# Optimization experiments

Measured on AMD Instinct MI355X. Metric: run time of the kernel, lower is better.

The kernel has to match this reference:

```python
import jax, jax.numpy as jnp
import numpy as np

COST_CLASS, COST_BBOX, COST_GIOU = 1.0, 5.0, 2.0
NUM_FRAMES, Q_PER_FRAME, NUM_TGT, NUM_CLASSES = 36, 100, 20, 92
B = 64


def box_cxcywh_to_xyxy(b):
    cx, cy, w, h = b[..., 0], b[..., 1], b[..., 2], b[..., 3]
    return jnp.stack([cx - 0.5 * w, cy - 0.5 * h, cx + 0.5 * w, cy + 0.5 * h], axis=-1)


def pairwise_giou(b1, b2):
    # b1: [..., Q, 4], b2: [..., T, 4], xyxy -> giou [..., Q, T]
    area1 = (b1[..., 2] - b1[..., 0]) * (b1[..., 3] - b1[..., 1])
    area2 = (b2[..., 2] - b2[..., 0]) * (b2[..., 3] - b2[..., 1])
    lt = jnp.maximum(b1[..., :, None, :2], b2[..., None, :, :2])
    rb = jnp.minimum(b1[..., :, None, 2:], b2[..., None, :, 2:])
    wh = jnp.clip(rb - lt, 0.0)
    inter = wh[..., 0] * wh[..., 1]
    union = area1[..., :, None] + area2[..., None, :] - inter
    iou = inter / union
    lt_e = jnp.minimum(b1[..., :, None, :2], b2[..., None, :, :2])
    rb_e = jnp.maximum(b1[..., :, None, 2:], b2[..., None, :, 2:])
    wh_e = jnp.clip(rb_e - lt_e, 0.0)
    area_e = wh_e[..., 0] * wh_e[..., 1]
    return iou - (area_e - union) / area_e


def compute_cost(pred_logits, pred_boxes, tgt_labels, tgt_boxes):
    b = pred_logits.shape[0]
    prob = jax.nn.softmax(pred_logits.reshape(b, NUM_FRAMES, Q_PER_FRAME, -1), axis=-1)  # [B,F,Q,C]
    pb = pred_boxes.reshape(b, NUM_FRAMES, Q_PER_FRAME, 4)
    lab = jnp.transpose(tgt_labels, (1, 0, 2))            # [B,F,T]
    tb = jnp.transpose(tgt_boxes, (1, 0, 2, 3))           # [B,F,T,4]
    onehot = jax.nn.one_hot(lab, prob.shape[-1], dtype=prob.dtype)  # [B,F,T,C]
    cost_class = -jnp.einsum('bfqc,bftc->bfqt', prob, onehot)
    cost_bbox = jnp.abs(pb[:, :, :, None, :] - tb[:, :, None, :, :]).sum(-1)  # L1 cdist
    giou = pairwise_giou(box_cxcywh_to_xyxy(pb), box_cxcywh_to_xyxy(tb))
    return COST_CLASS * cost_class + COST_BBOX * cost_bbox - COST_GIOU * giou


def auction_assign(cost):
    # cost [Q, T]; returns obj_of [T]: query index assigned to each target.
    # eps-optimal auction algorithm (replaces scipy linear_sum_assignment).
    Q, T = cost.shape
    benefit = -cost.T  # [T, Q]
    spread = jnp.max(benefit) - jnp.min(benefit) + 1e-6
    eps = spread / 1000.0
    neg_inf = jnp.asarray(-1e30, cost.dtype)

    def cond(s):
        _, _, obj_of, it = s
        return jnp.logical_and(jnp.any(obj_of < 0), it < 20000)

    def body(s):
        price, owner, obj_of, it = s
        unassigned = obj_of < 0                       # [T]
        vals = benefit - price[None, :]               # [T, Q]
        top2v, top2i = jax.lax.top_k(vals, 2)
        best_obj = top2i[:, 0]                        # [T]
        bid = price[best_obj] + (top2v[:, 0] - top2v[:, 1]) + eps
        bid = jnp.where(unassigned, bid, neg_inf)
        best_bid = jnp.full((Q,), neg_inf, cost.dtype).at[best_obj].max(bid)
        pids = jnp.arange(T, dtype=jnp.int32)
        win = unassigned & (bid >= best_bid[best_obj])
        winner = jnp.full((Q,), T, jnp.int32).at[best_obj].min(jnp.where(win, pids, T))
        has_bid = winner < T
        # evict previous owners of objects that received a bid
        evict = jnp.where(has_bid & (owner >= 0), owner, T)
        obj_of = obj_of.at[evict].set(-1, mode='drop')
        qids = jnp.arange(Q, dtype=jnp.int32)
        obj_of = obj_of.at[jnp.where(has_bid, winner, T)].set(jnp.where(has_bid, qids, -1), mode='drop')
        price = jnp.where(has_bid, best_bid, price)
        owner = jnp.where(has_bid, winner, owner)
        return price, owner, obj_of, it + 1

    init = (jnp.zeros((Q,), cost.dtype), jnp.full((Q,), -1, jnp.int32),
            jnp.full((T,), -1, jnp.int32), jnp.int32(0))
    _, _, obj_of, _ = jax.lax.while_loop(cond, body, init)
    return obj_of


def setup_inputs() -> dict:
    key = jax.random.key(0)
    k1, k2, k3, k4 = jax.random.split(key, 4)
    pred_logits = jax.random.normal(k1, (B, NUM_FRAMES * Q_PER_FRAME, NUM_CLASSES), jnp.float32)
    pred_boxes = jax.random.uniform(k2, (B, NUM_FRAMES * Q_PER_FRAME, 4), jnp.float32)
    tgt_labels = jax.random.randint(k3, (NUM_FRAMES, B, NUM_TGT), 0, NUM_CLASSES, jnp.int32)
    tgt_boxes = jax.random.uniform(k4, (NUM_FRAMES, B, NUM_TGT, 4), jnp.float32)
    return {'pred_logits': pred_logits, 'pred_boxes': pred_boxes,
            'tgt_labels': tgt_labels, 'tgt_boxes': tgt_boxes}


def reference(pred_logits, pred_boxes, tgt_labels, tgt_boxes):
    cost = compute_cost(pred_logits, pred_boxes, tgt_labels, tgt_boxes)  # [B,F,Q,T]
    b, f, q, t = cost.shape
    obj_of = jax.vmap(auction_assign)(cost.reshape(b * f, q, t))  # [BF, T]
    order = jnp.argsort(obj_of, axis=-1)  # scipy returns rows ascending
    pred_idx = jnp.take_along_axis(obj_of, order, axis=-1).reshape(b, f, t)
    tgt_idx = order.astype(jnp.int32).reshape(b, f, t)
    return cost, pred_idx, tgt_idx
```

## Files before the change

kernel.cpp:

```cpp
#include <hip/hip_runtime.h>

#define NF 36
#define QN 100
#define TN 20
#define CN 92
#define NB 64
#define BSTR 112

#define SCAN3(VV, IDX) do { \
    float v_ = (VV); \
    bool c0_ = v_ > v0; \
    bool c1_ = v_ > v1; \
    bool c2_ = v_ > v2; \
    i2 = c1_ ? i1 : (c2_ ? (IDX) : i2); \
    v2 = __builtin_amdgcn_fmed3f(v_, v1, v2); \
    i1 = c0_ ? i0 : (c1_ ? (IDX) : i1); \
    v1 = __builtin_amdgcn_fmed3f(v_, v0, v1); \
    i0 = c0_ ? (IDX) : i0; \
    v0 = fmaxf(v0, v_); } while (0)

#define CSWAP(VA,IA,BA,KA, VB,IB,BB,KB) do { \
    bool sw_ = ((VB) > (VA)) || (((VB) == (VA)) && ((IB) < (IA))); \
    float tv_ = sw_ ? (VB) : (VA); float uv_ = sw_ ? (VA) : (VB); (VA) = tv_; (VB) = uv_; \
    int   ti_ = sw_ ? (IB) : (IA); int   ui_ = sw_ ? (IA) : (IB); (IA) = ti_; (IB) = ui_; \
    float tb_ = sw_ ? (BB) : (BA); float ub_ = sw_ ? (BA) : (BB); (BA) = tb_; (BB) = ub_; \
    unsigned long long tk_ = sw_ ? (KB) : (KA); \
    unsigned long long uk_ = sw_ ? (KA) : (KB); (KA) = tk_; (KB) = uk_; \
} while (0)

__global__ __launch_bounds__(64) void matcher_kernel(
    const float* __restrict__ logits,
    const float* __restrict__ pboxes,
    const int*   __restrict__ tlabels,
    const float* __restrict__ tboxes,
    float* __restrict__ out_cost,
    float* __restrict__ out_pred,
    float* __restrict__ out_tgt)
{
    const int bf = blockIdx.x;
    const int b  = bf / NF;
    const int f  = bf % NF;
    const int lane = threadIdx.x;

    __shared__ __align__(16) float ben[TN][BSTR];
    __shared__ __align__(16) float price[BSTR];
    __shared__ unsigned long long pk[BSTR];
    __shared__ int   objl[TN];
    __shared__ int   slab[TN];
    __shared__ float tbr[TN][4];
    __shared__ float tbx[TN][4];
    __shared__ float tarea[TN];

    if (lane < TN) {
        const int base = (f * NB + b) * TN + lane;
        slab[lane] = tlabels[base];
        const float* tb = tboxes + (size_t)base * 4;
        float cx = tb[0], cy = tb[1], w = tb[2], h = tb[3];
        tbr[lane][0] = cx; tbr[lane][1] = cy; tbr[lane][2] = w; tbr[lane][3] = h;
        float x1 = cx - 0.5f * w, y1 = cy - 0.5f * h;
        float x2 = cx + 0.5f * w, y2 = cy + 0.5f * h;
        tbx[lane][0] = x1; tbx[lane][1] = y1; tbx[lane][2] = x2; tbx[lane][3] = y2;
        tarea[lane] = (x2 - x1) * (y2 - y1);
    }
    __syncthreads();

    float mn = INFINITY, mx = -INFINITY;
    for (int p = 0; p < 2; ++p) {
        const int q = lane + 64 * p;
        if (q < QN) {
            const size_t row = (size_t)b * (NF * QN) + (size_t)f * QN + q;
            const float* L = logits + row * CN;
            const float4* L4 = reinterpret_cast<const float4*>(L);
            float4 r[23];
            #pragma unroll
            for (int i = 0; i < 23; ++i) r[i] = L4[i];
            float m = -INFINITY;
            #pragma unroll
            for (int i = 0; i < 23; ++i) {
                float4 v = r[i];
                m = fmaxf(m, v.x); m = fmaxf(m, v.y); m = fmaxf(m, v.z); m = fmaxf(m, v.w);
            }
            float s = 0.f;
            #pragma unroll
            for (int i = 0; i < 23; ++i) {
                float4 v = r[i];
                s += expf(v.x - m); s += expf(v.y - m); s += expf(v.z - m); s += expf(v.w - m);
            }

            float4 pbv = reinterpret_cast<const float4*>(pboxes)[row];
            float cx = pbv.x, cy = pbv.y, w = pbv.z, h = pbv.w;
            float px1 = cx - 0.5f * w, py1 = cy - 0.5f * h;
            float px2 = cx + 0.5f * w, py2 = cy + 0.5f * h;
            float a1 = (px2 - px1) * (py2 - py1);

            for (int t = 0; t < TN; ++t) {
                float pc = expf(L[slab[t]] - m) / s;
                float cb = fabsf(cx - tbr[t][0]) + fabsf(cy - tbr[t][1]);
                cb = cb + fabsf(w - tbr[t][2]);
                cb = cb + fabsf(h - tbr[t][3]);
                float ltx = fmaxf(px1, tbx[t][0]), lty = fmaxf(py1, tbx[t][1]);
                float rbx = fminf(px2, tbx[t][2]), rby = fminf(py2, tbx[t][3]);
                float wx = fmaxf(rbx - ltx, 0.f), wy = fmaxf(rby - lty, 0.f);
                float inter = wx * wy;
                float uni = a1 + tarea[t] - inter;
                float iou = inter / uni;
                float ex1 = fminf(px1, tbx[t][0]), ey1 = fminf(py1, tbx[t][1]);
                float ex2 = fmaxf(px2, tbx[t][2]), ey2 = fmaxf(py2, tbx[t][3]);
                float ew = fmaxf(ex2 - ex1, 0.f), eh = fmaxf(ey2 - ey1, 0.f);
                float ae = ew * eh;
                float giou = iou - (ae - uni) / ae;
                float cost = (-pc) + 5.0f * cb - 2.0f * giou;
                ben[t][q] = -cost;
                mn = fminf(mn, cost);
                mx = fmaxf(mx, cost);
            }
        }
    }

    for (int i = lane; i < BSTR; i += 64) { price[i] = 0.f; pk[i] = 0ull; }
    if (lane < TN) {
        float4 ninf; ninf.x = ninf.y = ninf.z = ninf.w = -INFINITY;
        float4* sp = reinterpret_cast<float4*>(&ben[lane][100]);
        sp[0] = ninf; sp[1] = ninf; sp[2] = ninf;
    }
    __syncthreads();

    #pragma unroll
    for (int off = 32; off > 0; off >>= 1) {
        mn = fminf(mn, __shfl_xor(mn, off, 64));
        mx = fmaxf(mx, __shfl_xor(mx, off, 64));
    }
    const float eps = (((-mn) - (-mx)) + 1e-6f) / 1000.0f;

    {
        float4* dst = reinterpret_cast<float4*>(out_cost + (size_t)bf * (QN * TN));
        for (int i = lane; i < (QN * TN) / 4; i += 64) {
            int k = i * 4;
            int q = k / TN, t0 = k - q * TN;
            float4 v;
            v.x = -ben[t0 + 0][q]; v.y = -ben[t0 + 1][q];
            v.z = -ben[t0 + 2][q]; v.w = -ben[t0 + 3][q];
            dst[i] = v;
        }
    }

    const int myt = lane / 3;
    const int jj  = lane - myt * 3;
    const int q0  = jj * 36;
    const bool is_leader = (lane < 60) && (jj == 0);
    int myobj = -1;
    unsigned long long my_key = 0ull;

    float cv0 = 0.f, cv1 = 0.f, cv2 = 0.f, cb0 = 0.f, cb1 = 0.f, cb2 = 0.f, cB = 0.f;
    int ci0 = 0, ci1 = 0, ci2 = 0;
    unsigned long long ck0 = 0ull, ck1 = 0ull, ck2 = 0ull;
    bool cval = false;

    for (int it = 0; it < 20000; ++it) {
        if (is_leader) {
            if (myobj >= 0) {
                if (pk[myobj] != my_key) myobj = -1;
            }
            if (cval) {
                unsigned long long n0 = pk[ci0], n1 = pk[ci1], n2 = pk[ci2];
                bool ch0 = (n0 != ck0), ch1 = (n1 != ck1), ch2 = (n2 != ck2);
                if (ch0 | ch1 | ch2) {
                    if (ch0) { ck0 = n0; cv0 = cb0 - __uint_as_float((unsigned)(n0 >> 32)); }
                    if (ch1) { ck1 = n1; cv1 = cb1 - __uint_as_float((unsigned)(n1 >> 32)); }
                    if (ch2) { ck2 = n2; cv2 = cb2 - __uint_as_float((unsigned)(n2 >> 32)); }
                    CSWAP(cv0,ci0,cb0,ck0, cv1,ci1,cb1,ck1);
                    CSWAP(cv1,ci1,cb1,ck1, cv2,ci2,cb2,ck2);
                    CSWAP(cv0,ci0,cb0,ck0, cv1,ci1,cb1,ck1);
                    cval = (cv0 > cB) && (cv1 >= cB);
                }
            }
        }

        unsigned long long U = __ballot(is_leader && (myobj < 0));
        if (U == 0ull) break;
        unsigned long long R = __ballot(is_leader && (myobj < 0) && !cval);

        if (R != 0ull) {
            const bool doscan = (lane < 60) && (((R >> (3 * myt)) & 1ull) != 0ull);
            float v0 = -INFINITY, v1 = -INFINITY, v2 = -INFINITY;
            int i0 = q0, i1 = q0, i2 = q0;
            if (doscan) {
                const int tt = myt;
                const float4* pp = reinterpret_cast<const float4*>(&price[q0]);
                const float4* bp = reinterpret_cast<const float4*>(&ben[tt][q0]);
                #pragma unroll
                for (int k = 0; k < 9; ++k) {
                    float4 bv = bp[k];
                    float4 pv = pp[k];
                    SCAN3(bv.x - pv.x, q0 + 4*k + 0);
                    SCAN3(bv.y - pv.y, q0 + 4*k + 1);
                    SCAN3(bv.z - pv.z, q0 + 4*k + 2);
                    SCAN3(bv.w - pv.w, q0 + 4*k + 3);
                }
            }
            float sav0 = __shfl_down(v0, 1), sav1 = __shfl_down(v1, 1), sav2 = __shfl_down(v2, 1);
            int   sai0 = __shfl_down(i0, 1), sai1 = __shfl_down(i1, 1), sai2 = __shfl_down(i2, 1);
            float sbv0 = __shfl_down(v0, 2), sbv1 = __shfl_down(v1, 2), sbv2 = __shfl_down(v2, 2);
            int   sbi0 = __shfl_down(i0, 2), sbi1 = __shfl_down(i1, 2), sbi2 = __shfl_down(i2, 2);
            if (is_leader && (((R >> lane) & 1ull) != 0ull)) {
                SCAN3(sav0, sai0); SCAN3(sav1, sai1); SCAN3(sav2, sai2);
                SCAN3(sbv0, sbi0); SCAN3(sbv1, sbi1); SCAN3(sbv2, sbi2);
                ci0 = i0; ci1 = i1; ci2 = i2;
                cv0 = v0; cv1 = v1; cv2 = v2; cB = v2;
                cb0 = ben[myt][ci0]; cb1 = ben[myt][ci1]; cb2 = ben[myt][ci2];
                ck0 = pk[ci0]; ck1 = pk[ci1]; ck2 = pk[ci2];
                cval = true;
            }
        }

        const bool active = is_leader && (myobj < 0);
        if (active) {
            float cp0 = __uint_as_float((unsigned)(ck0 >> 32));
            float mybid = cp0 + (cv0 - cv1) + eps;
            unsigned long long mykey =
                ((unsigned long long)__float_as_uint(mybid) << 32) |
                (unsigned long long)(63 - myt);
            atomicMax(&pk[ci0], mykey);
            bool win;
            if ((U & (U - 1ull)) == 0ull) win = true;
            else win = (pk[ci0] == mykey);
            if (win) {
                myobj = ci0;
                my_key = mykey;
                price[ci0] = mybid;
            }
        }
    }
    __syncthreads();
    if (is_leader) objl[myt] = myobj;
    __syncthreads();

    if (lane < TN) {
        int v = objl[lane];
        int r = 0;
        for (int u2 = 0; u2 < TN; ++u2) {
            int w = objl[u2];
            r += (w < v) || (w == v && u2 < lane);
        }
        out_pred[(size_t)bf * TN + r] = (float)v;
        out_tgt[(size_t)bf * TN + r]  = (float)lane;
    }
}

extern "C" void kernel_launch(void* const* d_in, const int* in_sizes, int n_in,
                              void* d_out, int out_size, void* d_ws, size_t ws_size,
                              hipStream_t stream) {
    const float* logits  = (const float*)d_in[0];
    const float* pboxes  = (const float*)d_in[1];
    const int*   tlabels = (const int*)d_in[2];
    const float* tboxes  = (const float*)d_in[3];

    float* out = (float*)d_out;
    float* out_cost = out;
    float* out_pred = out + (size_t)NB * NF * QN * TN;
    float* out_tgt  = out_pred + (size_t)NB * NF * TN;

    hipLaunchKernelGGL(matcher_kernel, dim3(NB * NF), dim3(64), 0, stream,
                       logits, pboxes, tlabels, tboxes, out_cost, out_pred, out_tgt);
}
```

Before: 190.4 us.

## Resolve auction bids via wave-wide readlane broadcast instead of LDS atomics

```diff
diff --git a/kernel.cpp b/kernel.cpp
--- a/kernel.cpp
+++ b/kernel.cpp
@@ -19,16 +19,15 @@
     i0 = c0_ ? (IDX) : i0; \
     v0 = fmaxf(v0, v_); } while (0)
 
-#define CSWAP(VA,IA,BA,KA, VB,IB,BB,KB) do { \
+#define CSWAP(VA,IA,BA,PA, VB,IB,BB,PB) do { \
     bool sw_ = ((VB) > (VA)) || (((VB) == (VA)) && ((IB) < (IA))); \
     float tv_ = sw_ ? (VB) : (VA); float uv_ = sw_ ? (VA) : (VB); (VA) = tv_; (VB) = uv_; \
     int   ti_ = sw_ ? (IB) : (IA); int   ui_ = sw_ ? (IA) : (IB); (IA) = ti_; (IB) = ui_; \
     float tb_ = sw_ ? (BB) : (BA); float ub_ = sw_ ? (BA) : (BB); (BA) = tb_; (BB) = ub_; \
-    unsigned long long tk_ = sw_ ? (KB) : (KA); \
-    unsigned long long uk_ = sw_ ? (KA) : (KB); (KA) = tk_; (KB) = uk_; \
+    float tp_ = sw_ ? (PB) : (PA); float up_ = sw_ ? (PA) : (PB); (PA) = tp_; (PB) = up_; \
 } while (0)
 
-__global__ __launch_bounds__(64) void matcher_kernel(
+__global__ __launch_bounds__(64, 3) void matcher_kernel(
     const float* __restrict__ logits,
     const float* __restrict__ pboxes,
     const int*   __restrict__ tlabels,
@@ -44,7 +43,6 @@
 
     __shared__ __align__(16) float ben[TN][BSTR];
     __shared__ __align__(16) float price[BSTR];
-    __shared__ unsigned long long pk[BSTR];
     __shared__ int   objl[TN];
     __shared__ int   slab[TN];
     __shared__ float tbr[TN][4];
@@ -117,7 +115,7 @@
         }
     }
 
-    for (int i = lane; i < BSTR; i += 64) { price[i] = 0.f; pk[i] = 0ull; }
+    for (int i = lane; i < BSTR; i += 64) price[i] = 0.f;
     if (lane < TN) {
         float4 ninf; ninf.x = ninf.y = ninf.z = ninf.w = -INFINITY;
         float4* sp = reinterpret_cast<float4*>(&ben[lane][100]);
@@ -148,34 +146,22 @@
     const int jj  = lane - myt * 3;
     const int q0  = jj * 36;
     const bool is_leader = (lane < 60) && (jj == 0);
+    float4 breg4[9];
+    {
+        const int tt = (lane < 60) ? myt : 0;
+        const float4* bp = reinterpret_cast<const float4*>(&ben[tt][q0]);
+        #pragma unroll
+        for (int k = 0; k < 9; ++k) breg4[k] = bp[k];
+    }
     int myobj = -1;
-    unsigned long long my_key = 0ull;
-
-    float cv0 = 0.f, cv1 = 0.f, cv2 = 0.f, cb0 = 0.f, cb1 = 0.f, cb2 = 0.f, cB = 0.f;
+
+    float cv0 = 0.f, cv1 = 0.f, cv2 = 0.f;
+    float cb0 = 0.f, cb1 = 0.f, cb2 = 0.f;
+    float cp0 = 0.f, cp1 = 0.f, cp2 = 0.f, cB = 0.f;
     int ci0 = 0, ci1 = 0, ci2 = 0;
-    unsigned long long ck0 = 0ull, ck1 = 0ull, ck2 = 0ull;
     bool cval = false;
 
     for (int it = 0; it < 20000; ++it) {
-        if (is_leader) {
-            if (myobj >= 0) {
-                if (pk[myobj] != my_key) myobj = -1;
-            }
-            if (cval) {
-                unsigned long long n0 = pk[ci0], n1 = pk[ci1], n2 = pk[ci2];
-                bool ch0 = (n0 != ck0), ch1 = (n1 != ck1), ch2 = (n2 != ck2);
-                if (ch0 | ch1 | ch2) {
-                    if (ch0) { ck0 = n0; cv0 = cb0 - __uint_as_float((unsigned)(n0 >> 32)); }
-                    if (ch1) { ck1 = n1; cv1 = cb1 - __uint_as_float((unsigned)(n1 >> 32)); }
-                    if (ch2) { ck2 = n2; cv2 = cb2 - __uint_as_float((unsigned)(n2 >> 32)); }
-                    CSWAP(cv0,ci0,cb0,ck0, cv1,ci1,cb1,ck1);
-                    CSWAP(cv1,ci1,cb1,ck1, cv2,ci2,cb2,ck2);
-                    CSWAP(cv0,ci0,cb0,ck0, cv1,ci1,cb1,ck1);
-                    cval = (cv0 > cB) && (cv1 >= cB);
-                }
-            }
-        }
-
         unsigned long long U = __ballot(is_leader && (myobj < 0));
         if (U == 0ull) break;
         unsigned long long R = __ballot(is_leader && (myobj < 0) && !cval);
@@ -185,12 +171,10 @@
             float v0 = -INFINITY, v1 = -INFINITY, v2 = -INFINITY;
             int i0 = q0, i1 = q0, i2 = q0;
             if (doscan) {
-                const int tt = myt;
                 const float4* pp = reinterpret_cast<const float4*>(&price[q0]);
-                const float4* bp = reinterpret_cast<const float4*>(&ben[tt][q0]);
                 #pragma unroll
                 for (int k = 0; k < 9; ++k) {
-                    float4 bv = bp[k];
+                    float4 bv = breg4[k];
                     float4 pv = pp[k];
                     SCAN3(bv.x - pv.x, q0 + 4*k + 0);
                     SCAN3(bv.y - pv.y, q0 + 4*k + 1);
@@ -208,27 +192,46 @@
                 ci0 = i0; ci1 = i1; ci2 = i2;
                 cv0 = v0; cv1 = v1; cv2 = v2; cB = v2;
                 cb0 = ben[myt][ci0]; cb1 = ben[myt][ci1]; cb2 = ben[myt][ci2];
-                ck0 = pk[ci0]; ck1 = pk[ci1]; ck2 = pk[ci2];
+                cp0 = price[ci0];    cp1 = price[ci1];    cp2 = price[ci2];
                 cval = true;
             }
         }
 
         const bool active = is_leader && (myobj < 0);
-        if (active) {
-            float cp0 = __uint_as_float((unsigned)(ck0 >> 32));
-            float mybid = cp0 + (cv0 - cv1) + eps;
-            unsigned long long mykey =
-                ((unsigned long long)__float_as_uint(mybid) << 32) |
-                (unsigned long long)(63 - myt);
-            atomicMax(&pk[ci0], mykey);
-            bool win;
-            if ((U & (U - 1ull)) == 0ull) win = true;
-            else win = (pk[ci0] == mykey);
-            if (win) {
-                myobj = ci0;
-                my_key = mykey;
-                price[ci0] = mybid;
-            }
+        const float mybid  = cp0 + (cv0 - cv1) + eps;
+        const int   mybidq = ci0;
+
+        bool lose = false, ev = false, anyhit = false;
+        float np0 = cp0, np1 = cp1, np2 = cp2;
+        {
+            unsigned long long uu = U;
+            while (uu) {
+                const int pos = (int)__builtin_ctzll(uu); uu &= uu - 1ull;
+                const int t2  = pos / 3;
+                const int   q2 = __builtin_amdgcn_readlane(mybidq, pos);
+                const float f2 = __int_as_float(__builtin_amdgcn_readlane(__float_as_int(mybid), pos));
+                lose = lose || ((q2 == mybidq) && ((f2 > mybid) || ((f2 == mybid) && (t2 < myt))));
+                ev = ev || (q2 == myobj);
+                bool g0 = (q2 == ci0), g1 = (q2 == ci1), g2 = (q2 == ci2);
+                np0 = g0 ? fmaxf(np0, f2) : np0;
+                np1 = g1 ? fmaxf(np1, f2) : np1;
+                np2 = g2 ? fmaxf(np2, f2) : np2;
+                anyhit = anyhit || g0 || g1 || g2;
+            }
+        }
+        if (active && !lose) {
+            myobj = mybidq;
+            price[mybidq] = mybid;
+        } else if (ev) {
+            myobj = -1;
+        }
+        if (cval && anyhit) {
+            cp0 = np0; cp1 = np1; cp2 = np2;
+            cv0 = cb0 - cp0; cv1 = cb1 - cp1; cv2 = cb2 - cp2;
+            CSWAP(cv0,ci0,cb0,cp0, cv1,ci1,cb1,cp1);
+            CSWAP(cv1,ci1,cb1,cp1, cv2,ci2,cb2,cp2);
+            CSWAP(cv0,ci0,cb0,cp0, cv1,ci1,cb1,cp1);
+            cval = (cv0 > cB) && (cv1 >= cB);
         }
     }
     __syncthreads();
```

New measurement: 195.5 us. +2.7%, slower.
